# Kernel tuning notes

Hardware: AMD Instinct MI355X
Metric: run time of the kernel (lower is better)

Reference implementation:

```python
import jax, jax.numpy as jnp
import numpy as np

BN_EPS = 1e-5


def setup_inputs() -> dict:
    key = jax.random.key(0)
    k1, k2 = jax.random.split(key, 2)
    N_out, K, Cin, Cout = 65536, 8, 256, 512
    N_in = N_out * K
    data = jax.random.normal(k1, (N_in, Cin), dtype=jnp.float32)
    # Kaiming-ish scale for the conv weight [K*Cin, Cout]
    weight = jax.random.normal(k2, (K * Cin, Cout), dtype=jnp.float32) * (1.0 / np.sqrt(K * Cin))
    bias = jnp.zeros((Cout,), dtype=jnp.float32)
    gamma = jnp.ones((Cout,), dtype=jnp.float32)
    beta = jnp.zeros((Cout,), dtype=jnp.float32)
    # Full-octree stride-2 child indices: output node i gathers children 8i..8i+7
    neigh = jnp.arange(N_in, dtype=jnp.int64).reshape(N_out, K)
    return {"data": data, "weight": weight, "bias": bias,
            "gamma": gamma, "beta": beta, "neigh": neigh}


def reference(data, weight, bias, gamma, beta, neigh):
    # OctreeConv (kernel 2x2x2, stride 2, nempty): gather 8 children per output
    # node, then a single GEMM with weight [8*Cin, Cout].
    N_out, K = neigh.shape
    Cin = data.shape[1]
    feat = data[neigh.reshape(-1)].reshape(N_out, K * Cin)  # [N_out, 8*Cin]
    out = feat @ weight + bias                              # [N_out, Cout]
    # BatchNorm1d, training mode: biased batch stats over the node dim.
    mean = jnp.mean(out, axis=0)
    var = jnp.mean(jnp.square(out), axis=0) - jnp.square(mean)
    out = (out - mean) * jax.lax.rsqrt(var + BN_EPS) * gamma + beta
    return out
```

## Files before the change

kernel.cpp:

```cpp
#include <hip/hip_runtime.h>
#include <hip/hip_bf16.h>

typedef __attribute__((ext_vector_type(8))) short bf16x8;
typedef __attribute__((ext_vector_type(4))) float f32x4;

#define N_OUT 65536
#define CIN   256
#define COUT  512
#define BM    128
#define BN    256
#define BK    32
#define NKS   64

__device__ __forceinline__ unsigned short f2bf(float f) {
  union { __hip_bfloat16 h; unsigned short u; } c;
  c.h = __float2bfloat16(f);
  return c.u;
}

__device__ __forceinline__ bf16x8 pack8(f32x4 a, f32x4 b) {
  unsigned short u[8];
  u[0] = f2bf(a.x); u[1] = f2bf(a.y); u[2] = f2bf(a.z); u[3] = f2bf(a.w);
  u[4] = f2bf(b.x); u[5] = f2bf(b.y); u[6] = f2bf(b.z); u[7] = f2bf(b.w);
  return *reinterpret_cast<bf16x8*>(u);
}

__device__ __forceinline__ void gload_lds16f(const float* g, float* l) {
  __builtin_amdgcn_global_load_lds(
      (const __attribute__((address_space(1))) void*)g,
      (__attribute__((address_space(3))) void*)l, 16, 0, 0);
}
__device__ __forceinline__ void gload_lds16u(const unsigned short* g, unsigned short* l) {
  __builtin_amdgcn_global_load_lds(
      (const __attribute__((address_space(1))) void*)g,
      (__attribute__((address_space(3))) void*)l, 16, 0, 0);
}

__global__ void wprep_kernel(const float* __restrict__ W, unsigned short* __restrict__ Wt) {
  int idx = blockIdx.x * blockDim.x + threadIdx.x;
  if (idx >= 64 * 4 * COUT) return;
  int n  = idx & (COUT - 1);
  int s  = (idx >> 9) & 3;
  int kb = idx >> 11;
  unsigned short tmp[8];
#pragma unroll
  for (int w = 0; w < 8; ++w)
    tmp[w] = f2bf(W[(size_t)(kb * 32 + s * 8 + w) * COUT + n]);
  *reinterpret_cast<bf16x8*>(Wt + ((size_t)kb * 16384 + s * 4096 + n * 8)) =
      *reinterpret_cast<bf16x8*>(tmp);
}

__global__ __launch_bounds__(512, 4) void gemm_kernel(
    const float* __restrict__ data,
    const int*   __restrict__ neigh,
    const unsigned short* __restrict__ Wt,
    float* __restrict__ out,
    float* __restrict__ psum,
    float* __restrict__ psq)
{
  __shared__ union {
    struct {
      float          a[2][BM * BK];
      unsigned short b[2][BK * BN];
    } r;
    float st[8][BN];
  } sm;
  __shared__ unsigned int offs[BM * 8];

  const int tid = threadIdx.x;
  const int l   = tid & 63;
  const int w   = tid >> 6;
  const int wr  = w >> 1;
  const int wc  = w & 1;
  const int lg  = l >> 4;
  const int lm  = l & 15;

  const int bid = blockIdx.x;
  const int xcd = bid & 7;
  const int j   = bid >> 3;
  const int mb  = xcd * 64 + (j >> 1);
  const int nh  = j & 1;
  const int n0  = nh * BN;
  const int m0  = mb * BM;
  const int pidx = mb * 2 + nh;

  for (int e = tid; e < BM * 8; e += 512)
    offs[e] = ((unsigned)neigh[(size_t)m0 * 8 + e]) << 8;
  __syncthreads();

  f32x4 acc[2][8];
#pragma unroll
  for (int i = 0; i < 2; ++i)
#pragma unroll
    for (int jj = 0; jj < 8; ++jj) acc[i][jj] = (f32x4){0.f, 0.f, 0.f, 0.f};

  bf16x8 af[2];

  const int lrow = l >> 3;
  const int ra   = (w * 16 + lrow) * 8;
  const int rb   = (w * 16 + 8 + lrow) * 8;
  const int swzf = ((l & 7) ^ lrow) << 2;
  const int q0   = w * 2;
  const unsigned short* bbase =
      Wt + n0 * 8 + (q0 >> 2) * 4096 + (q0 & 3) * 512 + l * 8;

#define AISSUE(t_, buf_) do { \
    int cn_ = (t_) >> 3; \
    int k0_ = ((t_) & 7) * BK; \
    unsigned o0_ = offs[ra + cn_]; \
    unsigned o1_ = offs[rb + cn_]; \
    gload_lds16f(data + o0_ + k0_ + swzf, &sm.r.a[buf_][(w * 16) * BK]); \
    gload_lds16f(data + o1_ + k0_ + swzf, &sm.r.a[buf_][(w * 16 + 8) * BK]); \
  } while (0)

#define BISSUE(t_, buf_) do { \
    const unsigned short* bs_ = bbase + (size_t)(t_) * 16384; \
    gload_lds16u(bs_,       &sm.r.b[buf_][q0 * 512]); \
    gload_lds16u(bs_ + 512, &sm.r.b[buf_][q0 * 512 + 512]); \
  } while (0)

#define COMPUTE(buf_) do { \
    _Pragma("unroll") \
    for (int mi_ = 0; mi_ < 2; ++mi_) { \
      int R_ = wr * 32 + mi_ * 16 + lm; \
      const f32x4* ap_ = reinterpret_cast<const f32x4*>(&sm.r.a[buf_][R_ * BK]); \
      f32x4 x0_ = ap_[(2 * lg)     ^ (R_ & 7)]; \
      f32x4 x1_ = ap_[(2 * lg + 1) ^ (R_ & 7)]; \
      af[mi_] = pack8(x0_, x1_); \
    } \
    _Pragma("unroll") \
    for (int ni_ = 0; ni_ < 8; ++ni_) { \
      bf16x8 bfr_ = *reinterpret_cast<const bf16x8*>( \
          &sm.r.b[buf_][lg * 2048 + (wc * 128 + ni_ * 16 + lm) * 8]); \
      acc[0][ni_] = __builtin_amdgcn_mfma_f32_16x16x32_bf16(af[0], bfr_, acc[0][ni_], 0, 0, 0); \
      acc[1][ni_] = __builtin_amdgcn_mfma_f32_16x16x32_bf16(af[1], bfr_, acc[1][ni_], 0, 0, 0); \
    } \
  } while (0)

  AISSUE(0, 0); BISSUE(0, 0);
  AISSUE(1, 1); BISSUE(1, 1);

#pragma unroll 1
  for (int t = 0; t < NKS; ++t) {
    if (t < NKS - 1) asm volatile("s_waitcnt vmcnt(4)" ::: "memory");
    else             asm volatile("s_waitcnt vmcnt(0)" ::: "memory");
    __builtin_amdgcn_s_barrier();
    asm volatile("" ::: "memory");
    COMPUTE(t & 1);
    asm volatile("" ::: "memory");
    __builtin_amdgcn_s_barrier();
    if (t + 2 < NKS) { AISSUE(t + 2, t & 1); BISSUE(t + 2, t & 1); }
  }

#pragma unroll
  for (int mi = 0; mi < 2; ++mi) {
#pragma unroll
    for (int r = 0; r < 4; ++r) {
      size_t row = (size_t)(m0 + wr * 32 + mi * 16 + lg * 4 + r);
      float* op = out + row * COUT + n0 + wc * 128 + lm;
#pragma unroll
      for (int ni = 0; ni < 8; ++ni) op[ni * 16] = acc[mi][ni][r];
    }
  }

  __syncthreads();
#pragma unroll
  for (int ni = 0; ni < 8; ++ni) {
    float s1 = 0.f, s2 = 0.f;
#pragma unroll
    for (int mi = 0; mi < 2; ++mi)
#pragma unroll
      for (int r = 0; r < 4; ++r) { float v = acc[mi][ni][r]; s1 += v; s2 += v * v; }
    s1 += __shfl_xor(s1, 16, 64); s1 += __shfl_xor(s1, 32, 64);
    s2 += __shfl_xor(s2, 16, 64); s2 += __shfl_xor(s2, 32, 64);
    if (l < 16) {
      sm.st[wr][wc * 128 + ni * 16 + l]     = s1;
      sm.st[4 + wr][wc * 128 + ni * 16 + l] = s2;
    }
  }
  __syncthreads();
  if (tid < 256) {
    float S = sm.st[0][tid] + sm.st[1][tid] + sm.st[2][tid] + sm.st[3][tid];
    psum[(size_t)pidx * BN + tid] = S;
  } else {
    int c = tid - 256;
    float Q = sm.st[4][c] + sm.st[5][c] + sm.st[6][c] + sm.st[7][c];
    psq[(size_t)pidx * BN + c] = Q;
  }
#undef AISSUE
#undef BISSUE
#undef COMPUTE
}

__global__ void reduce1_kernel(const float* __restrict__ psum, const float* __restrict__ psq,
                               float* __restrict__ p2) {
  int c = threadIdx.x, b = blockIdx.x;
  int h = c >> 8, crel = c & 255;
  float s = 0.f, q = 0.f;
#pragma unroll
  for (int jj = 0; jj < 8; ++jj) {
    size_t pi = (size_t)((b * 8 + jj) * 2 + h);
    s += psum[pi * 256 + crel];
    q += psq [pi * 256 + crel];
  }
  p2[b * 1024 + c] = s;
  p2[b * 1024 + 512 + c] = q;
}

__global__ void reduce2_kernel(const float* __restrict__ p2,
                               const float* __restrict__ gamma,
                               const float* __restrict__ beta,
                               float* __restrict__ scsh) {
  int c = threadIdx.x;
  float s = 0.f, q = 0.f;
  for (int b = 0; b < 64; ++b) { s += p2[b * 1024 + c]; q += p2[b * 1024 + 512 + c]; }
  float mean = s * (1.f / 65536.f);
  float var  = q * (1.f / 65536.f) - mean * mean;
  float rs   = rsqrtf(var + 1e-5f);
  float sc   = gamma[c] * rs;
  scsh[c] = sc;
  scsh[COUT + c] = beta[c] - mean * sc;
}

__global__ void bn_kernel(float* __restrict__ out, const float* __restrict__ scsh) {
  __shared__ float sc[COUT], sh[COUT];
  int t = threadIdx.x;
  sc[t] = scsh[t];
  sh[t] = scsh[COUT + t];
  __syncthreads();
  f32x4* o4 = reinterpret_cast<f32x4*>(out);
  const size_t total  = (size_t)N_OUT * COUT / 4;
  const size_t stride = (size_t)gridDim.x * blockDim.x;
  for (size_t i = (size_t)blockIdx.x * blockDim.x + t; i < total; i += stride) {
    f32x4 v = o4[i];
    int c = ((int)(i & 127)) * 4;
    v.x = v.x * sc[c]     + sh[c];
    v.y = v.y * sc[c + 1] + sh[c + 1];
    v.z = v.z * sc[c + 2] + sh[c + 2];
    v.w = v.w * sc[c + 3] + sh[c + 3];
    o4[i] = v;
  }
}

extern "C" void kernel_launch(void* const* d_in, const int* in_sizes, int n_in,
                              void* d_out, int out_size, void* d_ws, size_t ws_size,
                              hipStream_t stream) {
  const float* data   = (const float*)d_in[0];
  const float* weight = (const float*)d_in[1];
  const float* gamma  = (const float*)d_in[3];
  const float* beta   = (const float*)d_in[4];
  const int*   neigh  = (const int*)d_in[5];
  float* out = (float*)d_out;

  char* ws = (char*)d_ws;
  unsigned short* Wt = (unsigned short*)ws;
  float* psum = (float*)(ws + (2u << 20));
  float* psq  = (float*)(ws + (3u << 20));
  float* p2   = (float*)(ws + (4u << 20));
  float* scsh = (float*)(ws + (4u << 20) + (256u << 10));

  wprep_kernel<<<512, 256, 0, stream>>>(weight, Wt);
  gemm_kernel<<<1024, 512, 0, stream>>>(data, neigh, Wt, out, psum, psq);
  reduce1_kernel<<<64, 512, 0, stream>>>(psum, psq, p2);
  reduce2_kernel<<<1, 512, 0, stream>>>(p2, gamma, beta, scsh);
  bn_kernel<<<2048, 512, 0, stream>>>(out, scsh);
}
```

Before: 273.7 us.

## Halve GEMM N-tile, triple-buffer LDS, and interleave prefetch with split MFMA phases

Shrinks the GEMM block tile from 128x256 to 128x128, doubling the grid to 2048 blocks, and moves from double to triple LDS buffering. Prefetch for step t+2 is now issued in the middle of the compute step, and the MFMA work is split into two phases with barriers and s_setprio, so loads overlap compute and one barrier per step goes away. The cost is that every A tile (the gathered fp32 activations) is now loaded twice as often, one extra time per N quarter, which raises global traffic and fp32-to-bf16 conversion work, and more barriers per step are added.

```diff
diff --git a/kernel.cpp b/kernel.cpp
--- a/kernel.cpp
+++ b/kernel.cpp
@@ -8,7 +8,7 @@
 #define CIN   256
 #define COUT  512
 #define BM    128
-#define BN    256
+#define BNB   128
 #define BK    32
 #define NKS   64
 
@@ -60,10 +60,10 @@
 {
   __shared__ union {
     struct {
-      float          a[2][BM * BK];
-      unsigned short b[2][BK * BN];
+      float          a[3][BM * BK];
+      unsigned short b[3][BK * BNB];
     } r;
-    float st[8][BN];
+    struct { float S[4][BNB]; float Q[4][BNB]; } st;
   } sm;
   __shared__ unsigned int offs[BM * 8];
 
@@ -77,32 +77,29 @@
 
   const int bid = blockIdx.x;
   const int xcd = bid & 7;
-  const int j   = bid >> 3;
-  const int mb  = xcd * 64 + (j >> 1);
-  const int nh  = j & 1;
-  const int n0  = nh * BN;
+  const int jj  = bid >> 3;
+  const int mb  = xcd * 64 + (jj >> 2);
+  const int nq  = jj & 3;
+  const int n0  = nq * BNB;
   const int m0  = mb * BM;
-  const int pidx = mb * 2 + nh;
+  const int pidx = mb * 4 + nq;
 
   for (int e = tid; e < BM * 8; e += 512)
     offs[e] = ((unsigned)neigh[(size_t)m0 * 8 + e]) << 8;
   __syncthreads();
 
-  f32x4 acc[2][8];
+  f32x4 acc[2][4];
 #pragma unroll
   for (int i = 0; i < 2; ++i)
 #pragma unroll
-    for (int jj = 0; jj < 8; ++jj) acc[i][jj] = (f32x4){0.f, 0.f, 0.f, 0.f};
-
-  bf16x8 af[2];
+    for (int j2 = 0; j2 < 4; ++j2) acc[i][j2] = (f32x4){0.f, 0.f, 0.f, 0.f};
 
   const int lrow = l >> 3;
   const int ra   = (w * 16 + lrow) * 8;
   const int rb   = (w * 16 + 8 + lrow) * 8;
   const int swzf = ((l & 7) ^ lrow) << 2;
-  const int q0   = w * 2;
-  const unsigned short* bbase =
-      Wt + n0 * 8 + (q0 >> 2) * 4096 + (q0 & 3) * 512 + l * 8;
+  const unsigned short* bsrc0 = Wt + (w >> 1) * 4096 + n0 * 8 + (w & 1) * 512 + l * 8;
+  unsigned short* bdst_base;
 
 #define AISSUE(t_, buf_) do { \
     int cn_ = (t_) >> 3; \
@@ -114,42 +111,64 @@
   } while (0)
 
 #define BISSUE(t_, buf_) do { \
-    const unsigned short* bs_ = bbase + (size_t)(t_) * 16384; \
-    gload_lds16u(bs_,       &sm.r.b[buf_][q0 * 512]); \
-    gload_lds16u(bs_ + 512, &sm.r.b[buf_][q0 * 512 + 512]); \
+    gload_lds16u(bsrc0 + (size_t)(t_) * 16384, \
+                 &sm.r.b[buf_][(w >> 1) * 1024 + (w & 1) * 512]); \
   } while (0)
 
-#define COMPUTE(buf_) do { \
-    _Pragma("unroll") \
-    for (int mi_ = 0; mi_ < 2; ++mi_) { \
-      int R_ = wr * 32 + mi_ * 16 + lm; \
-      const f32x4* ap_ = reinterpret_cast<const f32x4*>(&sm.r.a[buf_][R_ * BK]); \
-      f32x4 x0_ = ap_[(2 * lg)     ^ (R_ & 7)]; \
-      f32x4 x1_ = ap_[(2 * lg + 1) ^ (R_ & 7)]; \
-      af[mi_] = pack8(x0_, x1_); \
-    } \
-    _Pragma("unroll") \
-    for (int ni_ = 0; ni_ < 8; ++ni_) { \
-      bf16x8 bfr_ = *reinterpret_cast<const bf16x8*>( \
-          &sm.r.b[buf_][lg * 2048 + (wc * 128 + ni_ * 16 + lm) * 8]); \
-      acc[0][ni_] = __builtin_amdgcn_mfma_f32_16x16x32_bf16(af[0], bfr_, acc[0][ni_], 0, 0, 0); \
-      acc[1][ni_] = __builtin_amdgcn_mfma_f32_16x16x32_bf16(af[1], bfr_, acc[1][ni_], 0, 0, 0); \
-    } \
+#define MFMA2(g_, bf0_, bf1_) do { \
+    acc[0][2*(g_)]   = __builtin_amdgcn_mfma_f32_16x16x32_bf16(af0, bf0_, acc[0][2*(g_)],   0, 0, 0); \
+    acc[1][2*(g_)]   = __builtin_amdgcn_mfma_f32_16x16x32_bf16(af1, bf0_, acc[1][2*(g_)],   0, 0, 0); \
+    acc[0][2*(g_)+1] = __builtin_amdgcn_mfma_f32_16x16x32_bf16(af0, bf1_, acc[0][2*(g_)+1], 0, 0, 0); \
+    acc[1][2*(g_)+1] = __builtin_amdgcn_mfma_f32_16x16x32_bf16(af1, bf1_, acc[1][2*(g_)+1], 0, 0, 0); \
   } while (0)
 
   AISSUE(0, 0); BISSUE(0, 0);
   AISSUE(1, 1); BISSUE(1, 1);
 
+  const int R0 = wr * 32 + lm;
+  const int R1 = wr * 32 + 16 + lm;
+
 #pragma unroll 1
   for (int t = 0; t < NKS; ++t) {
-    if (t < NKS - 1) asm volatile("s_waitcnt vmcnt(4)" ::: "memory");
+    if (t < NKS - 1) asm volatile("s_waitcnt vmcnt(3)" ::: "memory");
     else             asm volatile("s_waitcnt vmcnt(0)" ::: "memory");
     __builtin_amdgcn_s_barrier();
     asm volatile("" ::: "memory");
-    COMPUTE(t & 1);
+
+    const int cur = t % 3;
+    const int pre = (t + 2) % 3;
+
+    const f32x4* ap0 = reinterpret_cast<const f32x4*>(&sm.r.a[cur][R0 * BK]);
+    const f32x4* ap1 = reinterpret_cast<const f32x4*>(&sm.r.a[cur][R1 * BK]);
+    f32x4 x00 = ap0[(2 * lg)     ^ (R0 & 7)];
+    f32x4 x01 = ap0[(2 * lg + 1) ^ (R0 & 7)];
+    f32x4 x10 = ap1[(2 * lg)     ^ (R1 & 7)];
+    f32x4 x11 = ap1[(2 * lg + 1) ^ (R1 & 7)];
+    bf16x8 b0 = *reinterpret_cast<const bf16x8*>(
+        &sm.r.b[cur][lg * 1024 + (wc * 64 + 0 * 16 + lm) * 8]);
+    bf16x8 b1 = *reinterpret_cast<const bf16x8*>(
+        &sm.r.b[cur][lg * 1024 + (wc * 64 + 1 * 16 + lm) * 8]);
+    if (t + 2 < NKS) { AISSUE(t + 2, pre); BISSUE(t + 2, pre); }
+    __builtin_amdgcn_s_barrier();
+    asm volatile("s_waitcnt lgkmcnt(0)" ::: "memory");
+    __builtin_amdgcn_sched_barrier(0);
+    bf16x8 af0 = pack8(x00, x01);
+    bf16x8 af1 = pack8(x10, x11);
+    __builtin_amdgcn_s_setprio(1);
+    MFMA2(0, b0, b1);
+    __builtin_amdgcn_s_setprio(0);
+
+    bf16x8 b2 = *reinterpret_cast<const bf16x8*>(
+        &sm.r.b[cur][lg * 1024 + (wc * 64 + 2 * 16 + lm) * 8]);
+    bf16x8 b3 = *reinterpret_cast<const bf16x8*>(
+        &sm.r.b[cur][lg * 1024 + (wc * 64 + 3 * 16 + lm) * 8]);
+    __builtin_amdgcn_s_barrier();
+    asm volatile("s_waitcnt lgkmcnt(0)" ::: "memory");
+    __builtin_amdgcn_sched_barrier(0);
+    __builtin_amdgcn_s_setprio(1);
+    MFMA2(1, b2, b3);
+    __builtin_amdgcn_s_setprio(0);
     asm volatile("" ::: "memory");
-    __builtin_amdgcn_s_barrier();
-    if (t + 2 < NKS) { AISSUE(t + 2, t & 1); BISSUE(t + 2, t & 1); }
   }
 
 #pragma unroll
@@ -157,15 +176,15 @@
 #pragma unroll
     for (int r = 0; r < 4; ++r) {
       size_t row = (size_t)(m0 + wr * 32 + mi * 16 + lg * 4 + r);
-      float* op = out + row * COUT + n0 + wc * 128 + lm;
-#pragma unroll
-      for (int ni = 0; ni < 8; ++ni) op[ni * 16] = acc[mi][ni][r];
+      float* op = out + row * COUT + n0 + wc * 64 + lm;
+#pragma unroll
+      for (int ni = 0; ni < 4; ++ni) op[ni * 16] = acc[mi][ni][r];
     }
   }
 
   __syncthreads();
 #pragma unroll
-  for (int ni = 0; ni < 8; ++ni) {
+  for (int ni = 0; ni < 4; ++ni) {
     float s1 = 0.f, s2 = 0.f;
 #pragma unroll
     for (int mi = 0; mi < 2; ++mi)
@@ -174,34 +193,34 @@
     s1 += __shfl_xor(s1, 16, 64); s1 += __shfl_xor(s1, 32, 64);
     s2 += __shfl_xor(s2, 16, 64); s2 += __shfl_xor(s2, 32, 64);
     if (l < 16) {
-      sm.st[wr][wc * 128 + ni * 16 + l]     = s1;
-      sm.st[4 + wr][wc * 128 + ni * 16 + l] = s2;
+      sm.st.S[wr][wc * 64 + ni * 16 + l] = s1;
+      sm.st.Q[wr][wc * 64 + ni * 16 + l] = s2;
     }
   }
   __syncthreads();
-  if (tid < 256) {
-    float S = sm.st[0][tid] + sm.st[1][tid] + sm.st[2][tid] + sm.st[3][tid];
-    psum[(size_t)pidx * BN + tid] = S;
-  } else {
-    int c = tid - 256;
-    float Q = sm.st[4][c] + sm.st[5][c] + sm.st[6][c] + sm.st[7][c];
-    psq[(size_t)pidx * BN + c] = Q;
+  if (tid < BNB) {
+    float S = sm.st.S[0][tid] + sm.st.S[1][tid] + sm.st.S[2][tid] + sm.st.S[3][tid];
+    psum[(size_t)pidx * BNB + tid] = S;
+  } else if (tid < 2 * BNB) {
+    int c = tid - BNB;
+    float Q = sm.st.Q[0][c] + sm.st.Q[1][c] + sm.st.Q[2][c] + sm.st.Q[3][c];
+    psq[(size_t)pidx * BNB + c] = Q;
   }
 #undef AISSUE
 #undef BISSUE
-#undef COMPUTE
+#undef MFMA2
 }
 
 __global__ void reduce1_kernel(const float* __restrict__ psum, const float* __restrict__ psq,
                                float* __restrict__ p2) {
   int c = threadIdx.x, b = blockIdx.x;
-  int h = c >> 8, crel = c & 255;
+  int nq = c >> 7, crel = c & 127;
   float s = 0.f, q = 0.f;
 #pragma unroll
-  for (int jj = 0; jj < 8; ++jj) {
-    size_t pi = (size_t)((b * 8 + jj) * 2 + h);
-    s += psum[pi * 256 + crel];
-    q += psq [pi * 256 + crel];
+  for (int j2 = 0; j2 < 8; ++j2) {
+    size_t pi = (size_t)((b * 8 + j2) * 4 + nq);
+    s += psum[pi * 128 + crel];
+    q += psq [pi * 128 + crel];
   }
   p2[b * 1024 + c] = s;
   p2[b * 1024 + 512 + c] = q;
@@ -260,7 +279,7 @@
   float* scsh = (float*)(ws + (4u << 20) + (256u << 10));
 
   wprep_kernel<<<512, 256, 0, stream>>>(weight, Wt);
-  gemm_kernel<<<1024, 512, 0, stream>>>(data, neigh, Wt, out, psum, psq);
+  gemm_kernel<<<2048, 512, 0, stream>>>(data, neigh, Wt, out, psum, psq);
   reduce1_kernel<<<64, 512, 0, stream>>>(psum, psq, p2);
   reduce2_kernel<<<1, 512, 0, stream>>>(p2, gamma, beta, scsh);
   bn_kernel<<<2048, 512, 0, stream>>>(out, scsh);
```

After: 356.5 us. +30.3%, slower.

## Convert A tile to bf16 once via registers and use 64x64 warp tiles

Applied to the files above, without the earlier changes.

The A tile is no longer copied to LDS as fp32 by direct global-to-LDS loads and repacked by every warp. Each thread now loads fp32 into registers, converts to bf16 once and writes it to a padded LDS layout (row stride 40 halfwords). The warp layout changes from 4x2 to 2x4 with 4x4 MFMA tiles per warp, which raises fragment reuse and reduces LDS reads per MFMA. The cost is that register-staged A loads need explicit vmcnt waits, which weakens latency hiding, and register pressure goes up.

```diff
diff --git a/kernel.cpp b/kernel.cpp
--- a/kernel.cpp
+++ b/kernel.cpp
@@ -11,6 +11,7 @@
 #define BN    256
 #define BK    32
 #define NKS   64
+#define ALD   40
 
 __device__ __forceinline__ unsigned short f2bf(float f) {
   union { __hip_bfloat16 h; unsigned short u; } c;
@@ -25,11 +26,6 @@
   return *reinterpret_cast<bf16x8*>(u);
 }
 
-__device__ __forceinline__ void gload_lds16f(const float* g, float* l) {
-  __builtin_amdgcn_global_load_lds(
-      (const __attribute__((address_space(1))) void*)g,
-      (__attribute__((address_space(3))) void*)l, 16, 0, 0);
-}
 __device__ __forceinline__ void gload_lds16u(const unsigned short* g, unsigned short* l) {
   __builtin_amdgcn_global_load_lds(
       (const __attribute__((address_space(1))) void*)g,
@@ -60,18 +56,18 @@
 {
   __shared__ union {
     struct {
-      float          a[2][BM * BK];
+      unsigned short a[2][BM * ALD];
       unsigned short b[2][BK * BN];
     } r;
-    float st[8][BN];
+    struct { float S[2][BN]; float Q[2][BN]; } st;
   } sm;
   __shared__ unsigned int offs[BM * 8];
 
   const int tid = threadIdx.x;
   const int l   = tid & 63;
   const int w   = tid >> 6;
-  const int wr  = w >> 1;
-  const int wc  = w & 1;
+  const int wr  = w >> 2;
+  const int wc  = w & 3;
   const int lg  = l >> 4;
   const int lm  = l & 15;
 
@@ -88,107 +84,117 @@
     offs[e] = ((unsigned)neigh[(size_t)m0 * 8 + e]) << 8;
   __syncthreads();
 
-  f32x4 acc[2][8];
-#pragma unroll
-  for (int i = 0; i < 2; ++i)
-#pragma unroll
-    for (int jj = 0; jj < 8; ++jj) acc[i][jj] = (f32x4){0.f, 0.f, 0.f, 0.f};
-
-  bf16x8 af[2];
-
-  const int lrow = l >> 3;
-  const int ra   = (w * 16 + lrow) * 8;
-  const int rb   = (w * 16 + 8 + lrow) * 8;
-  const int swzf = ((l & 7) ^ lrow) << 2;
-  const int q0   = w * 2;
+  f32x4 acc[4][4];
+#pragma unroll
+  for (int i = 0; i < 4; ++i)
+#pragma unroll
+    for (int jj = 0; jj < 4; ++jj) acc[i][jj] = (f32x4){0.f, 0.f, 0.f, 0.f};
+
+  const int arow  = tid >> 2;
+  const int achk  = tid & 3;
+  const int arow8 = arow * 8;
+  f32x4 sa0, sa1;
+
+  const int q0 = w * 2;
   const unsigned short* bbase =
       Wt + n0 * 8 + (q0 >> 2) * 4096 + (q0 & 3) * 512 + l * 8;
 
-#define AISSUE(t_, buf_) do { \
+#define AG(t_) do { \
     int cn_ = (t_) >> 3; \
     int k0_ = ((t_) & 7) * BK; \
-    unsigned o0_ = offs[ra + cn_]; \
-    unsigned o1_ = offs[rb + cn_]; \
-    gload_lds16f(data + o0_ + k0_ + swzf, &sm.r.a[buf_][(w * 16) * BK]); \
-    gload_lds16f(data + o1_ + k0_ + swzf, &sm.r.a[buf_][(w * 16 + 8) * BK]); \
-  } while (0)
-
-#define BISSUE(t_, buf_) do { \
+    const f32x4* p_ = reinterpret_cast<const f32x4*>(data + offs[arow8 + cn_] + k0_ + achk * 8); \
+    sa0 = p_[0]; sa1 = p_[1]; \
+  } while (0)
+
+#define AW(buf_) do { \
+    *reinterpret_cast<bf16x8*>(&sm.r.a[buf_][arow * ALD + achk * 8]) = pack8(sa0, sa1); \
+  } while (0)
+
+#define BD(t_, buf_) do { \
     const unsigned short* bs_ = bbase + (size_t)(t_) * 16384; \
     gload_lds16u(bs_,       &sm.r.b[buf_][q0 * 512]); \
     gload_lds16u(bs_ + 512, &sm.r.b[buf_][q0 * 512 + 512]); \
   } while (0)
 
 #define COMPUTE(buf_) do { \
+    bf16x8 af_[4]; \
     _Pragma("unroll") \
-    for (int mi_ = 0; mi_ < 2; ++mi_) { \
-      int R_ = wr * 32 + mi_ * 16 + lm; \
-      const f32x4* ap_ = reinterpret_cast<const f32x4*>(&sm.r.a[buf_][R_ * BK]); \
-      f32x4 x0_ = ap_[(2 * lg)     ^ (R_ & 7)]; \
-      f32x4 x1_ = ap_[(2 * lg + 1) ^ (R_ & 7)]; \
-      af[mi_] = pack8(x0_, x1_); \
+    for (int mi_ = 0; mi_ < 4; ++mi_) { \
+      int R_ = wr * 64 + mi_ * 16 + lm; \
+      af_[mi_] = *reinterpret_cast<const bf16x8*>(&sm.r.a[buf_][R_ * ALD + lg * 8]); \
     } \
     _Pragma("unroll") \
-    for (int ni_ = 0; ni_ < 8; ++ni_) { \
+    for (int ni_ = 0; ni_ < 4; ++ni_) { \
       bf16x8 bfr_ = *reinterpret_cast<const bf16x8*>( \
-          &sm.r.b[buf_][lg * 2048 + (wc * 128 + ni_ * 16 + lm) * 8]); \
-      acc[0][ni_] = __builtin_amdgcn_mfma_f32_16x16x32_bf16(af[0], bfr_, acc[0][ni_], 0, 0, 0); \
-      acc[1][ni_] = __builtin_amdgcn_mfma_f32_16x16x32_bf16(af[1], bfr_, acc[1][ni_], 0, 0, 0); \
+          &sm.r.b[buf_][lg * 2048 + (wc * 64 + ni_ * 16 + lm) * 8]); \
+      _Pragma("unroll") \
+      for (int mi_ = 0; mi_ < 4; ++mi_) \
+        acc[mi_][ni_] = __builtin_amdgcn_mfma_f32_16x16x32_bf16(af_[mi_], bfr_, acc[mi_][ni_], 0, 0, 0); \
     } \
   } while (0)
 
-  AISSUE(0, 0); BISSUE(0, 0);
-  AISSUE(1, 1); BISSUE(1, 1);
+  AG(0);
+  asm volatile("s_waitcnt vmcnt(0)" ::: "memory");
+  AW(0); BD(0, 0);
+  AG(1);
+  asm volatile("s_waitcnt vmcnt(0)" ::: "memory");
+  AW(1); BD(1, 1);
+  AG(2);
 
 #pragma unroll 1
   for (int t = 0; t < NKS; ++t) {
-    if (t < NKS - 1) asm volatile("s_waitcnt vmcnt(4)" ::: "memory");
-    else             asm volatile("s_waitcnt vmcnt(0)" ::: "memory");
+    asm volatile("s_waitcnt lgkmcnt(0)" ::: "memory");
     __builtin_amdgcn_s_barrier();
     asm volatile("" ::: "memory");
     COMPUTE(t & 1);
     asm volatile("" ::: "memory");
     __builtin_amdgcn_s_barrier();
-    if (t + 2 < NKS) { AISSUE(t + 2, t & 1); BISSUE(t + 2, t & 1); }
-  }
-
-#pragma unroll
-  for (int mi = 0; mi < 2; ++mi) {
+    if (t + 2 < NKS) {
+      asm volatile("s_waitcnt vmcnt(0)" ::: "memory");
+      AW(t & 1);
+      BD(t + 2, t & 1);
+      if (t + 3 < NKS) AG(t + 3);
+    } else if (t == NKS - 2) {
+      asm volatile("s_waitcnt vmcnt(0)" ::: "memory");
+    }
+  }
+
+#pragma unroll
+  for (int mi = 0; mi < 4; ++mi) {
 #pragma unroll
     for (int r = 0; r < 4; ++r) {
-      size_t row = (size_t)(m0 + wr * 32 + mi * 16 + lg * 4 + r);
-      float* op = out + row * COUT + n0 + wc * 128 + lm;
-#pragma unroll
-      for (int ni = 0; ni < 8; ++ni) op[ni * 16] = acc[mi][ni][r];
+      size_t row = (size_t)(m0 + wr * 64 + mi * 16 + lg * 4 + r);
+      float* op = out + row * COUT + n0 + wc * 64 + lm;
+#pragma unroll
+      for (int ni = 0; ni < 4; ++ni) op[ni * 16] = acc[mi][ni][r];
     }
   }
 
   __syncthreads();
 #pragma unroll
-  for (int ni = 0; ni < 8; ++ni) {
+  for (int ni = 0; ni < 4; ++ni) {
     float s1 = 0.f, s2 = 0.f;
 #pragma unroll
-    for (int mi = 0; mi < 2; ++mi)
+    for (int mi = 0; mi < 4; ++mi)
 #pragma unroll
       for (int r = 0; r < 4; ++r) { float v = acc[mi][ni][r]; s1 += v; s2 += v * v; }
     s1 += __shfl_xor(s1, 16, 64); s1 += __shfl_xor(s1, 32, 64);
     s2 += __shfl_xor(s2, 16, 64); s2 += __shfl_xor(s2, 32, 64);
     if (l < 16) {
-      sm.st[wr][wc * 128 + ni * 16 + l]     = s1;
-      sm.st[4 + wr][wc * 128 + ni * 16 + l] = s2;
+      sm.st.S[wr][wc * 64 + ni * 16 + l] = s1;
+      sm.st.Q[wr][wc * 64 + ni * 16 + l] = s2;
     }
   }
   __syncthreads();
-  if (tid < 256) {
-    float S = sm.st[0][tid] + sm.st[1][tid] + sm.st[2][tid] + sm.st[3][tid];
-    psum[(size_t)pidx * BN + tid] = S;
+  if (tid < BN) {
+    psum[(size_t)pidx * BN + tid] = sm.st.S[0][tid] + sm.st.S[1][tid];
   } else {
-    int c = tid - 256;
-    float Q = sm.st[4][c] + sm.st[5][c] + sm.st[6][c] + sm.st[7][c];
-    psq[(size_t)pidx * BN + c] = Q;
-  }
-#undef AISSUE
-#undef BISSUE
+    int c = tid - BN;
+    psq[(size_t)pidx * BN + c] = sm.st.Q[0][c] + sm.st.Q[1][c];
+  }
+#undef AG
+#undef AW
+#undef BD
 #undef COMPUTE
 }
 
```

After: 330.2 us. 1.21x slower.
